# Kernel optimization log

Measured on AMD Instinct MI355X. Metric: run time of the kernel, lower is better.

The kernel has to match this reference:

```python
import jax, jax.numpy as jnp
import numpy as np

DIM = 384
H = 6
D = DIM // H
MLP = 4 * DIM
SCALE = D ** -0.5
LN_EPS = 1e-5


def _ln(x, w, b):
    m = jnp.mean(x, axis=-1, keepdims=True)
    v = jnp.mean((x - m) ** 2, axis=-1, keepdims=True)
    return (x - m) * jax.lax.rsqrt(v + LN_EPS) * w + b


def setup_inputs() -> dict:
    key = jax.random.key(0)
    ks = jax.random.split(key, 8)
    B, N = 8, 1024
    x = jax.random.normal(ks[0], (B, N, DIM), dtype=jnp.float32)
    # torch nn.Linear weights are [out, in]
    qkv_w = jax.random.normal(ks[1], (3 * DIM, DIM), dtype=jnp.float32) * (DIM ** -0.5)
    proj_w = jax.random.normal(ks[2], (DIM, DIM), dtype=jnp.float32) * (DIM ** -0.5)
    proj_b = jnp.zeros((DIM,), jnp.float32)
    # L2Q params, 'quadratic' init
    alpha = jnp.full((H, 1, 1), 0.125, jnp.float32)
    beta = jnp.full((H, 1, 1), 0.5, jnp.float32)
    gamma = jnp.zeros((H, 1, 1), jnp.float32)
    ln1_w = jnp.ones((DIM,), jnp.float32)
    ln1_b = jnp.zeros((DIM,), jnp.float32)
    ln2_w = jnp.ones((DIM,), jnp.float32)
    ln2_b = jnp.zeros((DIM,), jnp.float32)
    w1 = jax.random.normal(ks[3], (MLP, DIM), dtype=jnp.float32) * (DIM ** -0.5)
    b1 = jnp.zeros((MLP,), jnp.float32)
    w2 = jax.random.normal(ks[4], (DIM, MLP), dtype=jnp.float32) * (MLP ** -0.5)
    b2 = jnp.zeros((DIM,), jnp.float32)
    return {"x": x, "qkv_w": qkv_w, "proj_w": proj_w, "proj_b": proj_b,
            "alpha": alpha, "beta": beta, "gamma": gamma,
            "ln1_w": ln1_w, "ln1_b": ln1_b, "ln2_w": ln2_w, "ln2_b": ln2_b,
            "w1": w1, "b1": b1, "w2": w2, "b2": b2}


def reference(x, qkv_w, proj_w, proj_b, alpha, beta, gamma,
              ln1_w, ln1_b, ln2_w, ln2_b, w1, b1, w2, b2):
    B, N, C = x.shape
    # --- L2Q attention on LN(x) ---
    h = _ln(x, ln1_w, ln1_b)
    qkv = (h @ qkv_w.T).reshape(B, N, 3, H, D)
    q = qkv[:, :, 0].transpose(0, 2, 1, 3)  # [B,H,N,D]
    k = qkv[:, :, 1].transpose(0, 2, 1, 3)
    v = qkv[:, :, 2].transpose(0, 2, 1, 3)
    logits = jnp.einsum('bhnd,bhmd->bhnm', q, k) * SCALE
    attn = jax.nn.relu(alpha * logits ** 2 + beta * logits + gamma)
    attn = attn / (jnp.sum(attn, axis=-1, keepdims=True) + 1e-6)
    out = jnp.einsum('bhnm,bhmd->bhnd', attn, v)
    out = out.transpose(0, 2, 1, 3).reshape(B, N, C)
    x = x + out @ proj_w.T + proj_b
    # --- MLP on LN(x), exact GELU (torch default) ---
    h2 = _ln(x, ln2_w, ln2_b)
    m = jax.nn.gelu(h2 @ w1.T + b1, approximate=False)
    x = x + m @ w2.T + b2
    return x
```

## Files before the change

### kernel.cpp

```cpp
#include <hip/hip_runtime.h>
#include <hip/hip_bf16.h>
#include <math.h>

#define DIMC 384
#define NH 6
#define HD 64
#define MLPD 1536
#define BS 8
#define SEQ 1024
#define T_TOK (BS*SEQ)
#define TC ((size_t)T_TOK*DIMC)
#define QK_SCALE 0.125f

typedef __bf16 bf16;
typedef bf16 bf16x4 __attribute__((ext_vector_type(4)));
typedef bf16 bf16x8 __attribute__((ext_vector_type(8)));
typedef float floatx4 __attribute__((ext_vector_type(4)));

__device__ __forceinline__ void async_cp16(const void* gsrc, void* ldst) {
    __builtin_amdgcn_global_load_lds(
        (const __attribute__((address_space(1))) unsigned int*)gsrc,
        (__attribute__((address_space(3))) unsigned int*)ldst,
        16, 0, 0);
}

__global__ __launch_bounds__(256)
void cvt_all(const float* __restrict__ s0, const float* __restrict__ s1,
             const float* __restrict__ s2, const float* __restrict__ s3,
             bf16* __restrict__ dst) {
    int i = blockIdx.x * 256 + threadIdx.x;
    const int n0 = 110592, n1 = 36864, n2 = 147456;
    const float4* src; int j;
    if (i < n0)           { src = (const float4*)s0; j = i; }
    else if (i < n0+n1)   { src = (const float4*)s1; j = i - n0; }
    else if (i < n0+n1+n2){ src = (const float4*)s2; j = i - n0 - n1; }
    else                  { src = (const float4*)s3; j = i - n0 - n1 - n2; }
    float4 v = src[j];
    bf16x4 o; o[0] = (bf16)v.x; o[1] = (bf16)v.y; o[2] = (bf16)v.z; o[3] = (bf16)v.w;
    ((bf16x4*)dst)[i] = o;
}

__global__ __launch_bounds__(256)
void ln_kernel(const float* __restrict__ x, const float* __restrict__ w,
               const float* __restrict__ b, bf16* __restrict__ out) {
    int row = blockIdx.x * 4 + (threadIdx.x >> 6);
    int t = threadIdx.x & 63;
    const float* xr = x + (size_t)row * DIMC;
    float vals[6];
    float s = 0.f;
    #pragma unroll
    for (int i = 0; i < 6; i++) { vals[i] = xr[t + i*64]; s += vals[i]; }
    #pragma unroll
    for (int m = 32; m; m >>= 1) s += __shfl_xor(s, m);
    float mean = s * (1.0f / DIMC);
    float sq = 0.f;
    #pragma unroll
    for (int i = 0; i < 6; i++) { float d = vals[i] - mean; sq += d * d; }
    #pragma unroll
    for (int m = 32; m; m >>= 1) sq += __shfl_xor(sq, m);
    float rstd = rsqrtf(sq * (1.0f / DIMC) + 1e-5f);
    bf16* orow = out + (size_t)row * DIMC;
    #pragma unroll
    for (int i = 0; i < 6; i++) {
        int c = t + i*64;
        orow[c] = (bf16)((vals[i] - mean) * rstd * w[c] + b[c]);
    }
}

__global__ __launch_bounds__(256)
void ln2_fused(const float* __restrict__ x, const bf16* __restrict__ p0,
               const bf16* __restrict__ p1, const float* __restrict__ pb,
               const float* __restrict__ w, const float* __restrict__ b,
               float* __restrict__ x1, bf16* __restrict__ h) {
    int row = blockIdx.x * 4 + (threadIdx.x >> 6);
    int t = threadIdx.x & 63;
    size_t base = (size_t)row * DIMC;
    float vals[6];
    float s = 0.f;
    #pragma unroll
    for (int i = 0; i < 6; i++) {
        int c = t + i*64;
        float v = x[base + c] + (float)p0[base + c] + (float)p1[base + c] + pb[c];
        vals[i] = v; s += v;
    }
    #pragma unroll
    for (int m = 32; m; m >>= 1) s += __shfl_xor(s, m);
    float mean = s * (1.0f / DIMC);
    float sq = 0.f;
    #pragma unroll
    for (int i = 0; i < 6; i++) { float d = vals[i] - mean; sq += d * d; }
    #pragma unroll
    for (int m = 32; m; m >>= 1) sq += __shfl_xor(sq, m);
    float rstd = rsqrtf(sq * (1.0f / DIMC) + 1e-5f);
    #pragma unroll
    for (int i = 0; i < 6; i++) {
        int c = t + i*64;
        x1[base + c] = vals[i];
        h[base + c] = (bf16)((vals[i] - mean) * rstd * w[c] + b[c]);
    }
}

__global__ __launch_bounds__(256)
void reduce4(float* __restrict__ xo, const bf16* __restrict__ p0, const bf16* __restrict__ p1,
             const bf16* __restrict__ p2, const bf16* __restrict__ p3,
             const float* __restrict__ b2) {
    int i = blockIdx.x * 256 + threadIdx.x;
    float4 v = ((const float4*)xo)[i];
    int c = (i % 96) * 4;
    float4 bb = *(const float4*)(b2 + c);
    bf16x4 a0 = ((const bf16x4*)p0)[i], a1 = ((const bf16x4*)p1)[i];
    bf16x4 a2 = ((const bf16x4*)p2)[i], a3 = ((const bf16x4*)p3)[i];
    v.x += bb.x + (float)a0[0] + (float)a1[0] + (float)a2[0] + (float)a3[0];
    v.y += bb.y + (float)a0[1] + (float)a1[1] + (float)a2[1] + (float)a3[1];
    v.z += bb.z + (float)a0[2] + (float)a1[2] + (float)a2[2] + (float)a3[2];
    v.w += bb.w + (float)a0[3] + (float)a1[3] + (float)a2[3] + (float)a3[3];
    ((float4*)xo)[i] = v;
}

enum { EPI_NONE = 0, EPI_QKV = 1, EPI_GELU = 3 };

template<int EPI, int K, int KS, typename OutT>
__global__ __launch_bounds__(256)
void gemm_bt(const bf16* __restrict__ A, const bf16* __restrict__ W,
             const float* __restrict__ bias, OutT* out, int M, int N) {
    __shared__ __align__(16) bf16 Ash[128*32];
    __shared__ __align__(16) bf16 Bsh[128*32];
    constexpr int KB = K / KS;
    int tid = threadIdx.x;
    int lane = tid & 63, w = tid >> 6;
    int quad = lane >> 4, l16 = lane & 15;
    int rbase = blockIdx.y * 128 + (w >> 1) * 64;
    int cbase = blockIdx.x * 128 + (w & 1) * 64;
    int kbase = blockIdx.z * KB;
    int c1 = w * 64 + lane;
    int c2 = c1 + 256;
    const bf16* Ag1 = A + (size_t)(blockIdx.y*128 + (c1 >> 2)) * K + kbase + (c1 & 3) * 8;
    const bf16* Ag2 = A + (size_t)(blockIdx.y*128 + (c2 >> 2)) * K + kbase + (c2 & 3) * 8;
    const bf16* Wg1 = W + (size_t)(blockIdx.x*128 + (c1 >> 2)) * K + kbase + (c1 & 3) * 8;
    const bf16* Wg2 = W + (size_t)(blockIdx.x*128 + (c2 >> 2)) * K + kbase + (c2 & 3) * 8;
    bf16* As1 = Ash + c1 * 8;  bf16* As2 = Ash + c2 * 8;
    bf16* Bs1 = Bsh + c1 * 8;  bf16* Bs2 = Bsh + c2 * 8;

    int arow = (w >> 1) * 64;
    int brow = (w & 1) * 64;
    floatx4 acc[4][4] = {};
    #pragma unroll
    for (int kk = 0; kk < KB / 32; kk++) {
        __syncthreads();
        async_cp16(Ag1 + kk*32, As1);
        async_cp16(Ag2 + kk*32, As2);
        async_cp16(Wg1 + kk*32, Bs1);
        async_cp16(Wg2 + kk*32, Bs2);
        __syncthreads();
        bf16x8 a[4], bfr[4];
        #pragma unroll
        for (int tm = 0; tm < 4; tm++)
            a[tm] = *(const bf16x8*)&Ash[(arow + tm*16 + l16) * 32 + quad*8];
        #pragma unroll
        for (int tn = 0; tn < 4; tn++)
            bfr[tn] = *(const bf16x8*)&Bsh[(brow + tn*16 + l16) * 32 + quad*8];
        #pragma unroll
        for (int tm = 0; tm < 4; tm++)
            #pragma unroll
            for (int tn = 0; tn < 4; tn++)
                acc[tm][tn] = __builtin_amdgcn_mfma_f32_16x16x32_bf16(a[tm], bfr[tn], acc[tm][tn], 0, 0, 0);
    }

    #pragma unroll
    for (int tm = 0; tm < 4; tm++)
        #pragma unroll
        for (int tn = 0; tn < 4; tn++) {
            if constexpr (EPI == EPI_QKV) {
                int colb = cbase + tn*16 + l16;
                int which = colb / 384;
                int rowb = rbase + tm*16 + quad*4;
                int bb = rowb >> 10;
                if (which == 2) {
                    int rem = colb - 768;
                    int hh = rem >> 6, d = rem & 63;
                    int n = rowb & 1023;
                    bf16x4 pk;
                    #pragma unroll
                    for (int r = 0; r < 4; r++) pk[r] = (bf16)acc[tm][tn][r];
                    *(bf16x4*)((bf16*)out + 2*TC + (((size_t)(bb*NH + hh) * HD + d) << 10) + n) = pk;
                } else {
                    int rem = colb - which*384;
                    int hh = rem >> 6, d = rem & 63;
                    #pragma unroll
                    for (int r = 0; r < 4; r++) {
                        int n = (rowb & 1023) + r;
                        ((bf16*)out)[(size_t)which*TC + (((size_t)(bb*NH + hh) * SEQ + n) << 6) + d]
                            = (bf16)acc[tm][tn][r];
                    }
                }
            } else if constexpr (EPI == EPI_NONE) {
                OutT* ob = out + (size_t)blockIdx.z * M * N;
                #pragma unroll
                for (int r = 0; r < 4; r++) {
                    int row = rbase + tm*16 + quad*4 + r;
                    int col = cbase + tn*16 + l16;
                    ob[(size_t)row * N + col] = (OutT)acc[tm][tn][r];
                }
            } else {
                #pragma unroll
                for (int r = 0; r < 4; r++) {
                    int row = rbase + tm*16 + quad*4 + r;
                    int col = cbase + tn*16 + l16;
                    float v = acc[tm][tn][r] + bias[col];
                    v = 0.5f * v * (1.0f + erff(v * 0.70710678118f));
                    out[(size_t)row * N + col] = (OutT)v;
                }
            }
        }
}

__global__ __launch_bounds__(256, 2)
void attn_kernel(const bf16* __restrict__ q, const bf16* __restrict__ k,
                 const bf16* __restrict__ vt, const float* __restrict__ alpha,
                 const float* __restrict__ beta, const float* __restrict__ gamma,
                 bf16* __restrict__ attn_out) {
    __shared__ __align__(16) bf16 Psh[64][264];
    __shared__ float rsW[4][64];
    __shared__ float rs_final[64];

    int L = blockIdx.x;
    int xcd = L & 7, slot = L >> 3;
    int qt = slot & 15;
    int bh = xcd + ((slot >> 4) << 3);
    int bb = bh / NH, h = bh % NH;
    int q0 = qt * 64;
    int tid = threadIdx.x;
    int w = tid >> 6, lane = tid & 63, quad = lane >> 4, l16 = lane & 15;
    float av = alpha[h] * (QK_SCALE * QK_SCALE), bv = beta[h] * QK_SCALE, gv = gamma[h];
    const bf16* qb  = q  + (size_t)bh * SEQ * HD;
    const bf16* kb  = k  + (size_t)bh * SEQ * HD;
    const bf16* vtb = vt + (size_t)bh * HD * SEQ;

    floatx4 o[4] = {};
    float rsp[4] = {0.f, 0.f, 0.f, 0.f};

    bf16x8 kf[2][4];
    #pragma unroll
    for (int ks = 0; ks < 2; ks++)
        #pragma unroll
        for (int ksub = 0; ksub < 4; ksub++)
            kf[ks][ksub] = *(const bf16x8*)(kb + (size_t)(w*64 + ksub*16 + l16) * HD + ks*32 + quad*8);

    for (int c = 0; c < 4; c++) {
        #pragma unroll
        for (int qsub = 0; qsub < 4; qsub++) {
            bf16x8 qa0 = *(const bf16x8*)(qb + (size_t)(q0 + qsub*16 + l16) * HD + quad*8);
            bf16x8 qa1 = *(const bf16x8*)(qb + (size_t)(q0 + qsub*16 + l16) * HD + 32 + quad*8);
            floatx4 s[4] = {};
            #pragma unroll
            for (int ksub = 0; ksub < 4; ksub++)
                s[ksub] = __builtin_amdgcn_mfma_f32_16x16x32_bf16(kf[0][ksub], qa0, s[ksub], 0, 0, 0);
            #pragma unroll
            for (int ksub = 0; ksub < 4; ksub++)
                s[ksub] = __builtin_amdgcn_mfma_f32_16x16x32_bf16(kf[1][ksub], qa1, s[ksub], 0, 0, 0);
            #pragma unroll
            for (int ksub = 0; ksub < 4; ksub++) {
                bf16x4 p4;
                float rsum = 0.f;
                #pragma unroll
                for (int r = 0; r < 4; r++) {
                    float xx = s[ksub][r];
                    float p = fmaxf((av*xx + bv)*xx + gv, 0.f);
                    p4[r] = (bf16)p;
                    rsum += p;
                }
                rsp[qsub] += rsum;
                *(bf16x4*)&Psh[qsub*16 + l16][w*64 + ksub*16 + quad*4] = p4;
            }
        }
        __syncthreads();
        if (c < 3) {
            int kc = (c+1)*256 + w*64;
            #pragma unroll
            for (int ks = 0; ks < 2; ks++)
                #pragma unroll
                for (int ksub = 0; ksub < 4; ksub++)
                    kf[ks][ksub] = *(const bf16x8*)(kb + (size_t)(kc + ksub*16 + l16) * HD + ks*32 + quad*8);
        }
        const bf16* vrow = vtb + (size_t)(w*16 + l16) * SEQ + c*256;
        #pragma unroll
        for (int ksl = 0; ksl < 8; ksl++) {
            bf16x8 vf = *(const bf16x8*)(vrow + ksl*32 + quad*8);
            #pragma unroll
            for (int qsub = 0; qsub < 4; qsub++) {
                bf16x8 pf = *(const bf16x8*)&Psh[qsub*16 + l16][ksl*32 + quad*8];
                o[qsub] = __builtin_amdgcn_mfma_f32_16x16x32_bf16(pf, vf, o[qsub], 0, 0, 0);
            }
        }
        __syncthreads();
    }

    #pragma unroll
    for (int qsub = 0; qsub < 4; qsub++) {
        rsp[qsub] += __shfl_xor(rsp[qsub], 16);
        rsp[qsub] += __shfl_xor(rsp[qsub], 32);
    }
    if (quad == 0) {
        #pragma unroll
        for (int qsub = 0; qsub < 4; qsub++)
            rsW[w][qsub*16 + l16] = rsp[qsub];
    }
    __syncthreads();
    if (tid < 64)
        rs_final[tid] = rsW[0][tid] + rsW[1][tid] + rsW[2][tid] + rsW[3][tid] + 1e-6f;
    __syncthreads();

    #pragma unroll
    for (int qsub = 0; qsub < 4; qsub++)
        #pragma unroll
        for (int r = 0; r < 4; r++) {
            int ql = qsub*16 + quad*4 + r;
            float rv = rs_final[ql];
            int n = q0 + ql;
            attn_out[((size_t)(bb*SEQ + n)) * DIMC + h*HD + w*16 + l16] =
                (bf16)(o[qsub][r] / rv);
        }
}

extern "C" void kernel_launch(void* const* d_in, const int* in_sizes, int n_in,
                              void* d_out, int out_size, void* d_ws, size_t ws_size,
                              hipStream_t stream) {
    const float* x      = (const float*)d_in[0];
    const float* qkv_w  = (const float*)d_in[1];
    const float* proj_w = (const float*)d_in[2];
    const float* proj_b = (const float*)d_in[3];
    const float* alpha  = (const float*)d_in[4];
    const float* beta   = (const float*)d_in[5];
    const float* gamma  = (const float*)d_in[6];
    const float* ln1_w  = (const float*)d_in[7];
    const float* ln1_b  = (const float*)d_in[8];
    const float* ln2_w  = (const float*)d_in[9];
    const float* ln2_b  = (const float*)d_in[10];
    const float* w1     = (const float*)d_in[11];
    const float* b1     = (const float*)d_in[12];
    const float* w2     = (const float*)d_in[13];
    const float* b2     = (const float*)d_in[14];
    float* out = (float*)d_out;

    char* base = (char*)d_ws;
    bf16* wq_bf = (bf16*)base;
    bf16* wp_bf = wq_bf + 442368;
    bf16* w1_bf = wq_bf + 589824;
    bf16* w2_bf = wq_bf + 1179648;
    bf16* h      = (bf16*)(base + 3538944);
    bf16* qkv    = (bf16*)(base + 9830400);
    bf16* attn_o = (bf16*)(base + 28704768);
    bf16* m      = qkv;
    bf16* Pp     = (bf16*)(base + 34996224);
    bf16* Pm     = (bf16*)(base + 34996224);

    cvt_all<<<1728, 256, 0, stream>>>(qkv_w, proj_w, w1, w2, wq_bf);
    ln_kernel<<<T_TOK/4, 256, 0, stream>>>(x, ln1_w, ln1_b, h);
    gemm_bt<EPI_QKV, 384, 1, bf16><<<dim3(9, 64, 1), 256, 0, stream>>>(
        h, wq_bf, nullptr, qkv, T_TOK, 1152);
    attn_kernel<<<768, 256, 0, stream>>>(
        qkv, qkv + TC, qkv + 2*TC, alpha, beta, gamma, attn_o);
    gemm_bt<EPI_NONE, 384, 2, bf16><<<dim3(3, 64, 2), 256, 0, stream>>>(
        attn_o, wp_bf, nullptr, Pp, T_TOK, DIMC);
    ln2_fused<<<T_TOK/4, 256, 0, stream>>>(x, Pp, Pp + TC, proj_b, ln2_w, ln2_b, out, h);
    gemm_bt<EPI_GELU, 384, 1, bf16><<<dim3(12, 64, 1), 256, 0, stream>>>(
        h, w1_bf, b1, m, T_TOK, MLPD);
    gemm_bt<EPI_NONE, 1536, 4, bf16><<<dim3(3, 64, 4), 256, 0, stream>>>(
        m, w2_bf, nullptr, Pm, T_TOK, DIMC);
    reduce4<<<TC/4/256, 256, 0, stream>>>(out, Pm, Pm + TC, Pm + 2*TC, Pm + 3*TC, b2);
}
```

Baseline: 228.5 us.

## Fuse weight conversion with LN1 and prefetch V fragments in attention

Merges the weight-conversion kernel and the first LayerNorm kernel into one launch, dispatched by block index, to save a launch and let both run concurrently. In the attention kernel, V fragments for the next key chunk are loaded into registers ahead of time instead of being fetched inside the PV loop. The P tile padding changes from 264 to 260 columns, so P is now read from LDS as two 8-byte halves. The launch-bounds occupancy hint of 2 is dropped. The extra live registers for the prefetched V and the changed LDS access pattern could lower occupancy or add bank conflicts.

```diff
diff --git a/kernel.cpp b/kernel.cpp
--- a/kernel.cpp
+++ b/kernel.cpp
@@ -25,45 +25,45 @@
 }
 
 __global__ __launch_bounds__(256)
-void cvt_all(const float* __restrict__ s0, const float* __restrict__ s1,
-             const float* __restrict__ s2, const float* __restrict__ s3,
-             bf16* __restrict__ dst) {
-    int i = blockIdx.x * 256 + threadIdx.x;
-    const int n0 = 110592, n1 = 36864, n2 = 147456;
-    const float4* src; int j;
-    if (i < n0)           { src = (const float4*)s0; j = i; }
-    else if (i < n0+n1)   { src = (const float4*)s1; j = i - n0; }
-    else if (i < n0+n1+n2){ src = (const float4*)s2; j = i - n0 - n1; }
-    else                  { src = (const float4*)s3; j = i - n0 - n1 - n2; }
-    float4 v = src[j];
-    bf16x4 o; o[0] = (bf16)v.x; o[1] = (bf16)v.y; o[2] = (bf16)v.z; o[3] = (bf16)v.w;
-    ((bf16x4*)dst)[i] = o;
-}
-
-__global__ __launch_bounds__(256)
-void ln_kernel(const float* __restrict__ x, const float* __restrict__ w,
-               const float* __restrict__ b, bf16* __restrict__ out) {
-    int row = blockIdx.x * 4 + (threadIdx.x >> 6);
-    int t = threadIdx.x & 63;
-    const float* xr = x + (size_t)row * DIMC;
-    float vals[6];
-    float s = 0.f;
-    #pragma unroll
-    for (int i = 0; i < 6; i++) { vals[i] = xr[t + i*64]; s += vals[i]; }
-    #pragma unroll
-    for (int m = 32; m; m >>= 1) s += __shfl_xor(s, m);
-    float mean = s * (1.0f / DIMC);
-    float sq = 0.f;
-    #pragma unroll
-    for (int i = 0; i < 6; i++) { float d = vals[i] - mean; sq += d * d; }
-    #pragma unroll
-    for (int m = 32; m; m >>= 1) sq += __shfl_xor(sq, m);
-    float rstd = rsqrtf(sq * (1.0f / DIMC) + 1e-5f);
-    bf16* orow = out + (size_t)row * DIMC;
-    #pragma unroll
-    for (int i = 0; i < 6; i++) {
-        int c = t + i*64;
-        orow[c] = (bf16)((vals[i] - mean) * rstd * w[c] + b[c]);
+void prep_kernel(const float* __restrict__ s0, const float* __restrict__ s1,
+                 const float* __restrict__ s2, const float* __restrict__ s3,
+                 bf16* __restrict__ dst,
+                 const float* __restrict__ x, const float* __restrict__ lw,
+                 const float* __restrict__ lb, bf16* __restrict__ out) {
+    if (blockIdx.x < 1728) {
+        int i = blockIdx.x * 256 + threadIdx.x;
+        const int n0 = 110592, n1 = 36864, n2 = 147456;
+        const float4* src; int j;
+        if (i < n0)           { src = (const float4*)s0; j = i; }
+        else if (i < n0+n1)   { src = (const float4*)s1; j = i - n0; }
+        else if (i < n0+n1+n2){ src = (const float4*)s2; j = i - n0 - n1; }
+        else                  { src = (const float4*)s3; j = i - n0 - n1 - n2; }
+        float4 v = src[j];
+        bf16x4 o; o[0] = (bf16)v.x; o[1] = (bf16)v.y; o[2] = (bf16)v.z; o[3] = (bf16)v.w;
+        ((bf16x4*)dst)[i] = o;
+    } else {
+        int row = (blockIdx.x - 1728) * 4 + (threadIdx.x >> 6);
+        int t = threadIdx.x & 63;
+        const float* xr = x + (size_t)row * DIMC;
+        float vals[6];
+        float s = 0.f;
+        #pragma unroll
+        for (int i = 0; i < 6; i++) { vals[i] = xr[t + i*64]; s += vals[i]; }
+        #pragma unroll
+        for (int m = 32; m; m >>= 1) s += __shfl_xor(s, m);
+        float mean = s * (1.0f / DIMC);
+        float sq = 0.f;
+        #pragma unroll
+        for (int i = 0; i < 6; i++) { float d = vals[i] - mean; sq += d * d; }
+        #pragma unroll
+        for (int m = 32; m; m >>= 1) sq += __shfl_xor(sq, m);
+        float rstd = rsqrtf(sq * (1.0f / DIMC) + 1e-5f);
+        bf16* orow = out + (size_t)row * DIMC;
+        #pragma unroll
+        for (int i = 0; i < 6; i++) {
+            int c = t + i*64;
+            orow[c] = (bf16)((vals[i] - mean) * rstd * lw[c] + lb[c]);
+        }
     }
 }
 
@@ -214,12 +214,12 @@
         }
 }
 
-__global__ __launch_bounds__(256, 2)
+__global__ __launch_bounds__(256)
 void attn_kernel(const bf16* __restrict__ q, const bf16* __restrict__ k,
                  const bf16* __restrict__ vt, const float* __restrict__ alpha,
                  const float* __restrict__ beta, const float* __restrict__ gamma,
                  bf16* __restrict__ attn_out) {
-    __shared__ __align__(16) bf16 Psh[64][264];
+    __shared__ __align__(16) bf16 Psh[64][260];
     __shared__ float rsW[4][64];
     __shared__ float rs_final[64];
 
@@ -239,12 +239,16 @@
     floatx4 o[4] = {};
     float rsp[4] = {0.f, 0.f, 0.f, 0.f};
 
-    bf16x8 kf[2][4];
+    bf16x8 kf[2][4], vf[8];
     #pragma unroll
     for (int ks = 0; ks < 2; ks++)
         #pragma unroll
         for (int ksub = 0; ksub < 4; ksub++)
             kf[ks][ksub] = *(const bf16x8*)(kb + (size_t)(w*64 + ksub*16 + l16) * HD + ks*32 + quad*8);
+    const bf16* vrow = vtb + (size_t)(w*16 + l16) * SEQ;
+    #pragma unroll
+    for (int ksl = 0; ksl < 8; ksl++)
+        vf[ksl] = *(const bf16x8*)(vrow + ksl*32 + quad*8);
 
     for (int c = 0; c < 4; c++) {
         #pragma unroll
@@ -282,15 +286,21 @@
                 for (int ksub = 0; ksub < 4; ksub++)
                     kf[ks][ksub] = *(const bf16x8*)(kb + (size_t)(kc + ksub*16 + l16) * HD + ks*32 + quad*8);
         }
-        const bf16* vrow = vtb + (size_t)(w*16 + l16) * SEQ + c*256;
         #pragma unroll
         for (int ksl = 0; ksl < 8; ksl++) {
-            bf16x8 vf = *(const bf16x8*)(vrow + ksl*32 + quad*8);
             #pragma unroll
             for (int qsub = 0; qsub < 4; qsub++) {
-                bf16x8 pf = *(const bf16x8*)&Psh[qsub*16 + l16][ksl*32 + quad*8];
-                o[qsub] = __builtin_amdgcn_mfma_f32_16x16x32_bf16(pf, vf, o[qsub], 0, 0, 0);
+                bf16x4 plo = *(const bf16x4*)&Psh[qsub*16 + l16][ksl*32 + quad*8];
+                bf16x4 phi = *(const bf16x4*)&Psh[qsub*16 + l16][ksl*32 + quad*8 + 4];
+                bf16x8 pf = __builtin_shufflevector(plo, phi, 0, 1, 2, 3, 4, 5, 6, 7);
+                o[qsub] = __builtin_amdgcn_mfma_f32_16x16x32_bf16(pf, vf[ksl], o[qsub], 0, 0, 0);
             }
+        }
+        if (c < 3) {
+            const bf16* vr2 = vrow + (c+1)*256;
+            #pragma unroll
+            for (int ksl = 0; ksl < 8; ksl++)
+                vf[ksl] = *(const bf16x8*)(vr2 + ksl*32 + quad*8);
         }
         __syncthreads();
     }
@@ -354,8 +364,8 @@
     bf16* Pp     = (bf16*)(base + 34996224);
     bf16* Pm     = (bf16*)(base + 34996224);
 
-    cvt_all<<<1728, 256, 0, stream>>>(qkv_w, proj_w, w1, w2, wq_bf);
-    ln_kernel<<<T_TOK/4, 256, 0, stream>>>(x, ln1_w, ln1_b, h);
+    prep_kernel<<<1728 + T_TOK/4, 256, 0, stream>>>(
+        qkv_w, proj_w, w1, w2, wq_bf, x, ln1_w, ln1_b, h);
     gemm_bt<EPI_QKV, 384, 1, bf16><<<dim3(9, 64, 1), 256, 0, stream>>>(
         h, wq_bf, nullptr, qkv, T_TOK, 1152);
     attn_kernel<<<768, 256, 0, stream>>>(
```

Measured after the change: 225.3 us. Within noise of the previous version (-1.4%).
